# Optimization experiments

Hardware: AMD Instinct MI355X
Metric: run time of the kernel (lower is better)

## Reference

```python
import jax, jax.numpy as jnp
import numpy as np

N_NODES = 100000
N_EDGES = 1600000
IN_C, HID_C, OUT_C = 19, 128, 4


def setup_inputs() -> dict:
    key = jax.random.key(0)
    ks = jax.random.split(key, 8)
    x = jax.random.normal(ks[0], (N_NODES, IN_C), dtype=jnp.float32)
    edge_index = jax.random.randint(ks[1], (2, N_EDGES), 0, N_NODES, dtype=jnp.int64)
    def glorot(k, shape):
        lim = np.sqrt(6.0 / (shape[0] + shape[1]))
        return jax.random.uniform(k, shape, jnp.float32, -lim, lim)
    return {
        "x": x,
        "edge_index": edge_index,
        "w1_l": glorot(ks[2], (IN_C, HID_C)),
        "w1_r": glorot(ks[3], (IN_C, HID_C)),
        "b1": jnp.zeros((HID_C,), jnp.float32),
        "w2_l": glorot(ks[4], (HID_C, OUT_C)),
        "w2_r": glorot(ks[5], (HID_C, OUT_C)),
        "b2": jnp.zeros((OUT_C,), jnp.float32),
    }


def _sage_conv(x, edge_index, w_l, w_r, b):
    # PyG SAGEConv (mean aggr): out = mean_{j in N(i)} x_j @ w_l + x_i @ w_r + b
    src, dst = edge_index[0], edge_index[1]
    n = x.shape[0]
    msg = x[src]                                            # [E, C] gather
    agg = jax.ops.segment_sum(msg, dst, num_segments=n)     # [N, C] scatter-add
    cnt = jax.ops.segment_sum(jnp.ones((src.shape[0],), x.dtype), dst, num_segments=n)
    mean = agg / jnp.maximum(cnt, 1.0)[:, None]
    return mean @ w_l + x @ w_r + b


def reference(x, edge_index, w1_l, w1_r, b1, w2_l, w2_r, b2):
    h = _sage_conv(x, edge_index, w1_l, w1_r, b1)
    h = jax.nn.relu(h)
    # dropout omitted (eval/inference mode reference)
    out = _sage_conv(h, edge_index, w2_l, w2_r, b2)
    return jax.nn.log_softmax(out, axis=1)
```

## Files before the change

### kernel.cpp

```cpp
#include <hip/hip_runtime.h>
#include <math.h>


constexpr int N    = 100000;
constexpr int E    = 1600000;
constexpr int INC  = 19;
constexpr int HID  = 128;
constexpr int OUTC = 4;
constexpr int WS   = 52;

constexpr int BSH    = 8;
constexpr int BMASK  = 255;
constexpr int NBUK   = (N + 255) >> BSH;
constexpr int BCAP   = 6144;
constexpr int BA_BLK = 256;
constexpr int CHUNK  = (E + BA_BLK - 1) / BA_BLK;
constexpr int CPT    = (CHUNK + 255) / 256;

__device__ inline float bf2f(unsigned short u) {
    return __uint_as_float((unsigned)u << 16);
}

__device__ inline unsigned short f2bf(float f) {
    unsigned u = __float_as_uint(f);
    u += 0x7FFFu + ((u >> 16) & 1u);
    return (unsigned short)(u >> 16);
}

__global__ void detect_pack(const int* __restrict__ ei, int* __restrict__ flag,
                            int* __restrict__ gcnt,
                            const float* __restrict__ x, float* __restrict__ xp,
                            unsigned short* __restrict__ xph) {
    int tid = blockIdx.x * blockDim.x + threadIdx.x;
    if (tid < N * 20) {
        int node = tid / 20;
        int c    = tid - node * 20;
        float v = (c < INC) ? x[(size_t)node * INC + c] : 0.f;
        xp[tid] = v;
        xph[tid] = f2bf(v);
    }
    if (blockIdx.x == 0) {
        __shared__ int any;
        if (threadIdx.x == 0) any = 0;
        __syncthreads();
        for (int k = threadIdx.x; k < 512; k += 256) gcnt[k] = 0;
        int v = 0;
        for (int k = threadIdx.x; k < 1024; k += 256)
            v |= ei[2 * k + 1];
        if (v) atomicOr(&any, 1);
        __syncthreads();
        if (threadIdx.x == 0) *flag = (any == 0) ? 1 : 0;
    }
}

__global__ __launch_bounds__(256) void bin_kernel(const int* __restrict__ ei,
                                                  const int* __restrict__ flag,
                                                  int* __restrict__ gcnt,
                                                  unsigned* __restrict__ be) {
    __shared__ int cnt[NBUK];
    __shared__ int base[NBUK];
    int t = threadIdx.x;
    for (int k = t; k < NBUK; k += 256) cnt[k] = 0;
    __syncthreads();

    int is64 = *flag;
    int lo = blockIdx.x * CHUNK;
    int hi = lo + CHUNK; if (hi > E) hi = E;

    int dstv[CPT];
#pragma unroll
    for (int k = 0; k < CPT; ++k) {
        int e = lo + k * 256 + t;
        int dv = 0;
        if (e < hi) {
            dv = is64 ? ei[2 * E + 2 * e] : ei[E + e];
            atomicAdd(&cnt[dv >> BSH], 1);
        }
        dstv[k] = dv;
    }
    __syncthreads();

    for (int k = t; k < NBUK; k += 256) {
        base[k] = atomicAdd(&gcnt[k], cnt[k]);
        cnt[k] = 0;
    }
    __syncthreads();

#pragma unroll
    for (int k = 0; k < CPT; ++k) {
        int e = lo + k * 256 + t;
        if (e < hi) {
            int dst = dstv[k];
            int src = is64 ? ei[2 * e] : ei[e];
            int b = dst >> BSH;
            int r = atomicAdd(&cnt[b], 1);
            int pos = base[b] + r;
            if (pos < BCAP)
                be[(size_t)b * BCAP + pos] =
                    ((unsigned)(dst & BMASK) << 17) | (unsigned)src;
        }
    }
}

__global__ void scan_wt(const int* __restrict__ gcnt, int* __restrict__ gbase,
                        const float* __restrict__ w1l, const float* __restrict__ w1r,
                        const float* __restrict__ b1,  const float* __restrict__ w2l,
                        const float* __restrict__ w2r, float* __restrict__ WT) {
    __shared__ int sd[512];
    int t = threadIdx.x;
    int v = (t < NBUK) ? gcnt[t] : 0;
    sd[t] = v;
    __syncthreads();
    for (int off = 1; off < 512; off <<= 1) {
        int add = (t >= off) ? sd[t - off] : 0;
        __syncthreads();
        sd[t] += add;
        __syncthreads();
    }
    if (t < NBUK) gbase[t] = sd[t] - v;

    int o = t;
    if (o < HID) {
        float* w = WT + o * WS;
        for (int c = 0; c < INC; ++c) {
            w[c]      = w1l[c * HID + o];
            w[20 + c] = w1r[c * HID + o];
        }
        w[19] = 0.f;
        w[39] = 0.f;
        for (int k = 0; k < OUTC; ++k) {
            w[40 + k] = w2l[o * OUTC + k];
            w[44 + k] = w2r[o * OUTC + k];
        }
        w[48] = b1[o];
        w[49] = 0.f; w[50] = 0.f; w[51] = 0.f;
    }
}

__global__ __launch_bounds__(256) void bucket_csr(const unsigned* __restrict__ be,
                                                  const int* __restrict__ gcnt,
                                                  const int* __restrict__ gbase,
                                                  int* __restrict__ adj,
                                                  int* __restrict__ deg,
                                                  int* __restrict__ start) {
    __shared__ int hist[256];
    __shared__ int sloc[256];
    __shared__ int cur[256];
    int b = blockIdx.x;
    int t = threadIdx.x;

    hist[t] = 0;
    cur[t]  = 0;
    __syncthreads();

    int sz = gcnt[b]; if (sz > BCAP) sz = BCAP;
    const unsigned* bp = be + (size_t)b * BCAP;

    for (int i = t; i < sz; i += 256) {
        int dl = bp[i] >> 17;
        atomicAdd(&hist[dl], 1);
    }
    __syncthreads();

    int v = hist[t];
    sloc[t] = v;
    __syncthreads();
    for (int off = 1; off < 256; off <<= 1) {
        int add = (t >= off) ? sloc[t - off] : 0;
        __syncthreads();
        sloc[t] += add;
        __syncthreads();
    }
    int sl = sloc[t] - v;

    int gb = gbase[b];
    int node = b * 256 + t;
    if (node < N) {
        deg[node]   = v;
        start[node] = gb + sl;
    }
    __syncthreads();

    for (int i = t; i < sz; i += 256) {
        unsigned p = bp[i];
        int dl  = p >> 17;
        int src = (int)(p & 0x1FFFFu);
        int r = atomicAdd(&cur[dl], 1);
        adj[gb + (sloc[dl] - hist[dl]) + r] = src;
    }
}

__global__ void gather_bf16(const ushort4* __restrict__ xph4,
                            const int* __restrict__ adj,
                            const int* __restrict__ start,
                            const int* __restrict__ deg,
                            float4* __restrict__ mean1p4) {
    int tid = blockIdx.x * blockDim.x + threadIdx.x;
    if (tid >= N * 5) return;
    int node = tid / 5;
    int q    = tid - node * 5;
    int d  = deg[node];
    int st = start[node];
    float4 a0 = make_float4(0.f, 0.f, 0.f, 0.f);
    float4 a1 = a0, a2 = a0, a3 = a0;
    int j = 0;
    for (; j + 3 < d; j += 4) {
        int s0 = adj[st + j];
        int s1 = adj[st + j + 1];
        int s2 = adj[st + j + 2];
        int s3 = adj[st + j + 3];
        ushort4 u0 = xph4[(size_t)s0 * 5 + q];
        ushort4 u1 = xph4[(size_t)s1 * 5 + q];
        ushort4 u2 = xph4[(size_t)s2 * 5 + q];
        ushort4 u3 = xph4[(size_t)s3 * 5 + q];
        a0.x += bf2f(u0.x); a0.y += bf2f(u0.y); a0.z += bf2f(u0.z); a0.w += bf2f(u0.w);
        a1.x += bf2f(u1.x); a1.y += bf2f(u1.y); a1.z += bf2f(u1.z); a1.w += bf2f(u1.w);
        a2.x += bf2f(u2.x); a2.y += bf2f(u2.y); a2.z += bf2f(u2.z); a2.w += bf2f(u2.w);
        a3.x += bf2f(u3.x); a3.y += bf2f(u3.y); a3.z += bf2f(u3.z); a3.w += bf2f(u3.w);
    }
    for (; j < d; ++j) {
        ushort4 u = xph4[(size_t)adj[st + j] * 5 + q];
        a0.x += bf2f(u.x); a0.y += bf2f(u.y); a0.z += bf2f(u.z); a0.w += bf2f(u.w);
    }
    float inv = 1.0f / fmaxf((float)d, 1.0f);
    float4 m;
    m.x = ((a0.x + a1.x) + (a2.x + a3.x)) * inv;
    m.y = ((a0.y + a1.y) + (a2.y + a3.y)) * inv;
    m.z = ((a0.z + a1.z) + (a2.z + a3.z)) * inv;
    m.w = ((a0.w + a1.w) + (a2.w + a3.w)) * inv;
    mean1p4[(size_t)node * 5 + q] = m;
}

__global__ __launch_bounds__(256) void dense_v6(
        const float4* __restrict__ xp4,
        const float4* __restrict__ mean1p4,
        const float* __restrict__ WT,
        float* __restrict__ g,
        float* __restrict__ s) {
    __shared__ float P[3][64 * 9];

    int t    = threadIdx.x;
    int lane = t & 63;
    int part = __builtin_amdgcn_readfirstlane(t >> 6);
    int node = blockIdx.x * 64 + lane;
    bool valid = node < N;

    float msp[20], xsp[20];
#pragma unroll
    for (int q = 0; q < 5; ++q) {
        float4 mv = valid ? mean1p4[(size_t)node * 5 + q] : make_float4(0.f, 0.f, 0.f, 0.f);
        float4 xv = valid ? xp4[(size_t)node * 5 + q]     : make_float4(0.f, 0.f, 0.f, 0.f);
        msp[4 * q] = mv.x; msp[4 * q + 1] = mv.y; msp[4 * q + 2] = mv.z; msp[4 * q + 3] = mv.w;
        xsp[4 * q] = xv.x; xsp[4 * q + 1] = xv.y; xsp[4 * q + 2] = xv.z; xsp[4 * q + 3] = xv.w;
    }

    float r[8] = {0.f, 0.f, 0.f, 0.f, 0.f, 0.f, 0.f, 0.f};
    int o0 = part * 32;
#pragma unroll 2
    for (int oo = 0; oo < 32; ++oo) {
        int o = o0 + oo;
        const float* __restrict__ w = WT + o * WS;
        float a0 = 0.f, a1 = 0.f, a2 = 0.f, a3 = 0.f;
#pragma unroll
        for (int q = 0; q < 5; ++q) {
            a0 += msp[4 * q]     * w[4 * q]      + xsp[4 * q]     * w[20 + 4 * q];
            a1 += msp[4 * q + 1] * w[4 * q + 1]  + xsp[4 * q + 1] * w[21 + 4 * q];
            a2 += msp[4 * q + 2] * w[4 * q + 2]  + xsp[4 * q + 2] * w[22 + 4 * q];
            a3 += msp[4 * q + 3] * w[4 * q + 3]  + xsp[4 * q + 3] * w[23 + 4 * q];
        }
        float h = fmaxf(((a0 + a1) + (a2 + a3)) + w[48], 0.0f);
        r[0] += h * w[40]; r[1] += h * w[41]; r[2] += h * w[42]; r[3] += h * w[43];
        r[4] += h * w[44]; r[5] += h * w[45]; r[6] += h * w[46]; r[7] += h * w[47];
    }

    if (part != 0) {
        float* p = &P[part - 1][lane * 9];
#pragma unroll
        for (int k = 0; k < 8; ++k) p[k] = r[k];
    }
    __syncthreads();

    if (part == 0 && valid) {
#pragma unroll
        for (int k = 0; k < 8; ++k)
            r[k] = ((r[k] + P[0][lane * 9 + k]) + P[1][lane * 9 + k])
                   + P[2][lane * 9 + k];
        *(float4*)(g + (size_t)node * OUTC) = make_float4(r[0], r[1], r[2], r[3]);
        *(float4*)(s + (size_t)node * OUTC) = make_float4(r[4], r[5], r[6], r[7]);
    }
}

__global__ void final_v3(const float* __restrict__ g,
                         const int* __restrict__ adj,
                         const int* __restrict__ start,
                         const int* __restrict__ deg,
                         const float* __restrict__ s,
                         const float* __restrict__ b2,
                         float* __restrict__ out) {
    int tid  = blockIdx.x * blockDim.x + threadIdx.x;
    int node = tid >> 2;
    int l    = tid & 3;
    if (node >= N) return;
    int d  = deg[node];
    int st = start[node];
    float ax = 0.f, ay = 0.f, az = 0.f, aw = 0.f;
    for (int j = l; j < d; j += 4) {
        int sn = adj[st + j];
        const float4 gv = *(const float4*)(g + (size_t)sn * OUTC);
        ax += gv.x; ay += gv.y; az += gv.z; aw += gv.w;
    }
    ax += __shfl_down(ax, 2, 4); ay += __shfl_down(ay, 2, 4);
    az += __shfl_down(az, 2, 4); aw += __shfl_down(aw, 2, 4);
    ax += __shfl_down(ax, 1, 4); ay += __shfl_down(ay, 1, 4);
    az += __shfl_down(az, 1, 4); aw += __shfl_down(aw, 1, 4);
    if (l == 0) {
        float inv = 1.0f / fmaxf((float)d, 1.0f);
        const float4 sv = *(const float4*)(s + (size_t)node * OUTC);
        float o0 = ax * inv + sv.x + b2[0];
        float o1 = ay * inv + sv.y + b2[1];
        float o2 = az * inv + sv.z + b2[2];
        float o3 = aw * inv + sv.w + b2[3];
        float m = fmaxf(fmaxf(o0, o1), fmaxf(o2, o3));
        float sum = expf(o0 - m) + expf(o1 - m) + expf(o2 - m) + expf(o3 - m);
        float lse = logf(sum) + m;
        *(float4*)(out + (size_t)node * OUTC) =
            make_float4(o0 - lse, o1 - lse, o2 - lse, o3 - lse);
    }
}

extern "C" void kernel_launch(void* const* d_in, const int* in_sizes, int n_in,
                              void* d_out, int out_size, void* d_ws, size_t ws_size,
                              hipStream_t stream) {
    const float* x   = (const float*)d_in[0];
    const int*   ei  = (const int*)d_in[1];
    const float* w1l = (const float*)d_in[2];
    const float* w1r = (const float*)d_in[3];
    const float* b1  = (const float*)d_in[4];
    const float* w2l = (const float*)d_in[5];
    const float* w2r = (const float*)d_in[6];
    const float* b2  = (const float*)d_in[7];
    float* out = (float*)d_out;

    int*            ws    = (int*)d_ws;
    int*            flag  = ws;
    int*            gcnt  = ws + 64;
    int*            gbase = gcnt + 512;
    int*            deg   = gbase + 512;
    int*            start = deg + N;
    unsigned*       be    = (unsigned*)(start + N);
    int*            adj   = (int*)(be + (size_t)NBUK * BCAP);
    float*          g     = (float*)(adj + E);
    float*          s     = g + (size_t)N * OUTC;
    float*          xp    = s + (size_t)N * OUTC;
    unsigned short* xph   = (unsigned short*)(xp + (size_t)N * 20);
    float*          mean1p= (float*)(xph + (size_t)N * 20);
    float*          WT    = mean1p + (size_t)N * 20;

    detect_pack<<<(N * 20 + 255) / 256, 256, 0, stream>>>(ei, flag, gcnt, x, xp, xph);
    bin_kernel<<<BA_BLK, 256, 0, stream>>>(ei, flag, gcnt, be);
    scan_wt<<<1, 512, 0, stream>>>(gcnt, gbase, w1l, w1r, b1, w2l, w2r, WT);
    bucket_csr<<<NBUK, 256, 0, stream>>>(be, gcnt, gbase, adj, deg, start);
    gather_bf16<<<(N * 5 + 255) / 256, 256, 0, stream>>>(
        (const ushort4*)xph, adj, start, deg, (float4*)mean1p);
    dense_v6<<<(N + 63) / 64, 256, 0, stream>>>(
        (const float4*)xp, (const float4*)mean1p, WT, g, s);
    final_v3<<<(N * 4 + 255) / 256, 256, 0, stream>>>(g, adj, start, deg, s, b2, out);
}
```

Baseline: 116.1 us.

## Drop scan kernel: fold weight transpose into pack, compute bucket offsets inline

Removes the single-block scan_wt launch. The weight transpose moves into block 1 of detect_pack, and each bucket_csr block computes its own global base by summing the preceding bucket counts through a shared atomic. The gather loop is also unrolled to 8 neighbours per iteration so more loads are in flight. This saves one launch and a serial scan step, at the cost of a redundant O(NBUK) prefix read in every bucket block.

After: 112.3 us. -3.3%, faster.

```diff
diff --git a/kernel.cpp b/kernel.cpp
--- a/kernel.cpp
+++ b/kernel.cpp
@@ -30,7 +30,10 @@
 __global__ void detect_pack(const int* __restrict__ ei, int* __restrict__ flag,
                             int* __restrict__ gcnt,
                             const float* __restrict__ x, float* __restrict__ xp,
-                            unsigned short* __restrict__ xph) {
+                            unsigned short* __restrict__ xph,
+                            const float* __restrict__ w1l, const float* __restrict__ w1r,
+                            const float* __restrict__ b1,  const float* __restrict__ w2l,
+                            const float* __restrict__ w2r, float* __restrict__ WT) {
     int tid = blockIdx.x * blockDim.x + threadIdx.x;
     if (tid < N * 20) {
         int node = tid / 20;
@@ -50,6 +53,23 @@
         if (v) atomicOr(&any, 1);
         __syncthreads();
         if (threadIdx.x == 0) *flag = (any == 0) ? 1 : 0;
+    } else if (blockIdx.x == 1) {
+        int o = threadIdx.x;
+        if (o < HID) {
+            float* w = WT + o * WS;
+            for (int c = 0; c < INC; ++c) {
+                w[c]      = w1l[c * HID + o];
+                w[20 + c] = w1r[c * HID + o];
+            }
+            w[19] = 0.f;
+            w[39] = 0.f;
+            for (int k = 0; k < OUTC; ++k) {
+                w[40 + k] = w2l[o * OUTC + k];
+                w[44 + k] = w2r[o * OUTC + k];
+            }
+            w[48] = b1[o];
+            w[49] = 0.f; w[50] = 0.f; w[51] = 0.f;
+        }
     }
 }
 
@@ -102,56 +122,26 @@
     }
 }
 
-__global__ void scan_wt(const int* __restrict__ gcnt, int* __restrict__ gbase,
-                        const float* __restrict__ w1l, const float* __restrict__ w1r,
-                        const float* __restrict__ b1,  const float* __restrict__ w2l,
-                        const float* __restrict__ w2r, float* __restrict__ WT) {
-    __shared__ int sd[512];
-    int t = threadIdx.x;
-    int v = (t < NBUK) ? gcnt[t] : 0;
-    sd[t] = v;
-    __syncthreads();
-    for (int off = 1; off < 512; off <<= 1) {
-        int add = (t >= off) ? sd[t - off] : 0;
-        __syncthreads();
-        sd[t] += add;
-        __syncthreads();
-    }
-    if (t < NBUK) gbase[t] = sd[t] - v;
-
-    int o = t;
-    if (o < HID) {
-        float* w = WT + o * WS;
-        for (int c = 0; c < INC; ++c) {
-            w[c]      = w1l[c * HID + o];
-            w[20 + c] = w1r[c * HID + o];
-        }
-        w[19] = 0.f;
-        w[39] = 0.f;
-        for (int k = 0; k < OUTC; ++k) {
-            w[40 + k] = w2l[o * OUTC + k];
-            w[44 + k] = w2r[o * OUTC + k];
-        }
-        w[48] = b1[o];
-        w[49] = 0.f; w[50] = 0.f; w[51] = 0.f;
-    }
-}
-
 __global__ __launch_bounds__(256) void bucket_csr(const unsigned* __restrict__ be,
                                                   const int* __restrict__ gcnt,
-                                                  const int* __restrict__ gbase,
                                                   int* __restrict__ adj,
                                                   int* __restrict__ deg,
                                                   int* __restrict__ start) {
     __shared__ int hist[256];
     __shared__ int sloc[256];
     __shared__ int cur[256];
+    __shared__ int gbs;
     int b = blockIdx.x;
     int t = threadIdx.x;
 
     hist[t] = 0;
     cur[t]  = 0;
-    __syncthreads();
+    if (t == 0) gbs = 0;
+    __syncthreads();
+
+    int part = 0;
+    for (int i = t; i < b; i += 256) part += gcnt[i];
+    if (part) atomicAdd(&gbs, part);
 
     int sz = gcnt[b]; if (sz > BCAP) sz = BCAP;
     const unsigned* bp = be + (size_t)b * BCAP;
@@ -173,7 +163,7 @@
     }
     int sl = sloc[t] - v;
 
-    int gb = gbase[b];
+    int gb = gbs;
     int node = b * 256 + t;
     if (node < N) {
         deg[node]   = v;
@@ -204,6 +194,32 @@
     float4 a0 = make_float4(0.f, 0.f, 0.f, 0.f);
     float4 a1 = a0, a2 = a0, a3 = a0;
     int j = 0;
+    for (; j + 7 < d; j += 8) {
+        int s0 = adj[st + j];
+        int s1 = adj[st + j + 1];
+        int s2 = adj[st + j + 2];
+        int s3 = adj[st + j + 3];
+        int s4 = adj[st + j + 4];
+        int s5 = adj[st + j + 5];
+        int s6 = adj[st + j + 6];
+        int s7 = adj[st + j + 7];
+        ushort4 u0 = xph4[(size_t)s0 * 5 + q];
+        ushort4 u1 = xph4[(size_t)s1 * 5 + q];
+        ushort4 u2 = xph4[(size_t)s2 * 5 + q];
+        ushort4 u3 = xph4[(size_t)s3 * 5 + q];
+        ushort4 u4 = xph4[(size_t)s4 * 5 + q];
+        ushort4 u5 = xph4[(size_t)s5 * 5 + q];
+        ushort4 u6 = xph4[(size_t)s6 * 5 + q];
+        ushort4 u7 = xph4[(size_t)s7 * 5 + q];
+        a0.x += bf2f(u0.x); a0.y += bf2f(u0.y); a0.z += bf2f(u0.z); a0.w += bf2f(u0.w);
+        a1.x += bf2f(u1.x); a1.y += bf2f(u1.y); a1.z += bf2f(u1.z); a1.w += bf2f(u1.w);
+        a2.x += bf2f(u2.x); a2.y += bf2f(u2.y); a2.z += bf2f(u2.z); a2.w += bf2f(u2.w);
+        a3.x += bf2f(u3.x); a3.y += bf2f(u3.y); a3.z += bf2f(u3.z); a3.w += bf2f(u3.w);
+        a0.x += bf2f(u4.x); a0.y += bf2f(u4.y); a0.z += bf2f(u4.z); a0.w += bf2f(u4.w);
+        a1.x += bf2f(u5.x); a1.y += bf2f(u5.y); a1.z += bf2f(u5.z); a1.w += bf2f(u5.w);
+        a2.x += bf2f(u6.x); a2.y += bf2f(u6.y); a2.z += bf2f(u6.z); a2.w += bf2f(u6.w);
+        a3.x += bf2f(u7.x); a3.y += bf2f(u7.y); a3.z += bf2f(u7.z); a3.w += bf2f(u7.w);
+    }
     for (; j + 3 < d; j += 4) {
         int s0 = adj[st + j];
         int s1 = adj[st + j + 1];
@@ -344,8 +360,7 @@
     int*            ws    = (int*)d_ws;
     int*            flag  = ws;
     int*            gcnt  = ws + 64;
-    int*            gbase = gcnt + 512;
-    int*            deg   = gbase + 512;
+    int*            deg   = gcnt + 512;
     int*            start = deg + N;
     unsigned*       be    = (unsigned*)(start + N);
     int*            adj   = (int*)(be + (size_t)NBUK * BCAP);
@@ -356,10 +371,10 @@
     float*          mean1p= (float*)(xph + (size_t)N * 20);
     float*          WT    = mean1p + (size_t)N * 20;
 
-    detect_pack<<<(N * 20 + 255) / 256, 256, 0, stream>>>(ei, flag, gcnt, x, xp, xph);
+    detect_pack<<<(N * 20 + 255) / 256, 256, 0, stream>>>(
+        ei, flag, gcnt, x, xp, xph, w1l, w1r, b1, w2l, w2r, WT);
     bin_kernel<<<BA_BLK, 256, 0, stream>>>(ei, flag, gcnt, be);
-    scan_wt<<<1, 512, 0, stream>>>(gcnt, gbase, w1l, w1r, b1, w2l, w2r, WT);
-    bucket_csr<<<NBUK, 256, 0, stream>>>(be, gcnt, gbase, adj, deg, start);
+    bucket_csr<<<NBUK, 256, 0, stream>>>(be, gcnt, adj, deg, start);
     gather_bf16<<<(N * 5 + 255) / 256, 256, 0, stream>>>(
         (const ushort4*)xph, adj, start, deg, (float4*)mean1p);
     dense_v6<<<(N + 63) / 64, 256, 0, stream>>>(
```
